# Kernel tuning notes

Hardware: AMD Instinct MI355X
Metric: run time of the kernel (lower is better)

Reference implementation:

```python
import jax, jax.numpy as jnp
import numpy as np

HEADS = 20
HEAD_DIM = 64  # 1280 / 20
IP_SCALE = 1.0


def _split_heads(x, B):
    # [B, S, H*D] -> [B, H, S, D]
    return x.reshape(B, -1, HEADS, HEAD_DIM).transpose(0, 2, 1, 3)


def _merge_heads(x, B):
    # [B, H, S, D] -> [B, S, H*D]
    return x.transpose(0, 2, 1, 3).reshape(B, -1, HEADS * HEAD_DIM)


def _sdpa(q, k, v):
    # q:[B,H,Sq,D] k,v:[B,H,Sk,D]
    scale = 1.0 / jnp.sqrt(jnp.asarray(HEAD_DIM, q.dtype))
    scores = jnp.einsum('bhqd,bhkd->bhqk', q, k) * scale
    probs = jax.nn.softmax(scores, axis=-1)
    return jnp.einsum('bhqk,bhkd->bhqd', probs, v)


def setup_inputs() -> dict:
    key = jax.random.key(0)
    ks = jax.random.split(key, 10)
    B, S, D = 8, 4096, 1280
    Ctx, Cdim = 77, 2048
    Adim = 768
    inp = {
        'hidden_states': jax.random.normal(ks[0], (B, S, D), jnp.float32),
        'encoder_hidden_states': jax.random.normal(ks[1], (B, Ctx, Cdim), jnp.float32),
        'adapter_embeds': jax.random.normal(ks[2], (B, 1, Adim), jnp.float32),
        'Wq': jax.random.normal(ks[3], (D, D), jnp.float32) * 0.02,
        'Wk': jax.random.normal(ks[4], (Cdim, D), jnp.float32) * 0.02,
        'Wv': jax.random.normal(ks[5], (Cdim, D), jnp.float32) * 0.02,
        'Wk_adapter': jax.random.normal(ks[6], (Adim, D), jnp.float32) * 0.02,
        'Wv_adapter': jax.random.normal(ks[7], (Adim, D), jnp.float32) * 0.02,
        'Wo': jax.random.normal(ks[8], (D, D), jnp.float32) * 0.02,
        'bo': jnp.zeros((D,), jnp.float32),
    }
    return inp


def reference(hidden_states, encoder_hidden_states, adapter_embeds,
              Wq, Wk, Wv, Wk_adapter, Wv_adapter, Wo, bo):
    B = hidden_states.shape[0]

    # base cross-attention projections
    q = _split_heads(hidden_states @ Wq, B)                 # [B,H,S,D]
    k = _split_heads(encoder_hidden_states @ Wk, B)         # [B,H,77,D]
    v = _split_heads(encoder_hidden_states @ Wv, B)
    out = _merge_heads(_sdpa(q, k, v), B)                   # [B,S,H*D]

    # IP-adapter branch: single-token K/V, shares the same query
    k_ip = _split_heads(adapter_embeds @ Wk_adapter, B)     # [B,H,1,D]
    v_ip = _split_heads(adapter_embeds @ Wv_adapter, B)
    out_ip = _merge_heads(_sdpa(q, k_ip, v_ip), B)

    merged = out + IP_SCALE * out_ip
    return merged @ Wo + bo
```

## Files before the change

### kernel.cpp

```cpp
#include <hip/hip_runtime.h>
#include <hip/hip_bf16.h>
#include <cstdint>
#include <cstddef>

typedef __hip_bfloat16 bf16_t;
typedef __attribute__((ext_vector_type(8))) __bf16 bf16x8;
typedef __attribute__((ext_vector_type(4))) float f32x4;

__device__ __forceinline__ void gld_lds16(const void* g, void* l) {
    __builtin_amdgcn_global_load_lds(
        (const __attribute__((address_space(1))) void*)(g),
        (__attribute__((address_space(3))) void*)(l), 16, 0, 0);
}

__global__ void k_cast(const float* __restrict__ in, bf16_t* __restrict__ out, long n) {
    long i = ((long)blockIdx.x * blockDim.x + threadIdx.x) * 4;
    if (i >= n) return;
    float4 v = *(const float4*)(in + i);
    out[i + 0] = __float2bfloat16(v.x);
    out[i + 1] = __float2bfloat16(v.y);
    out[i + 2] = __float2bfloat16(v.z);
    out[i + 3] = __float2bfloat16(v.w);
}

__global__ void k_cast_pad(const float* __restrict__ in, bf16_t* __restrict__ out,
                           int rows_in, int rows_out, int cols) {
    long i = ((long)blockIdx.x * blockDim.x + threadIdx.x) * 4;
    long n = (long)rows_out * cols;
    if (i >= n) return;
    int r = (int)(i / cols);
    if (r < rows_in) {
        float4 v = *(const float4*)(in + i);
        out[i + 0] = __float2bfloat16(v.x);
        out[i + 1] = __float2bfloat16(v.y);
        out[i + 2] = __float2bfloat16(v.z);
        out[i + 3] = __float2bfloat16(v.w);
    } else {
        bf16_t z = __float2bfloat16(0.f);
        out[i + 0] = z; out[i + 1] = z; out[i + 2] = z; out[i + 3] = z;
    }
}

__global__ void k_transpose_cast(const float* __restrict__ in, bf16_t* __restrict__ out,
                                 int R, int C) {
    __shared__ float tile[32][33];
    int bx = blockIdx.x * 32;
    int by = blockIdx.y * 32;
    int tx = threadIdx.x & 31, ty = threadIdx.x >> 5;
    #pragma unroll
    for (int j = 0; j < 32; j += 8)
        tile[ty + j][tx] = in[(size_t)(by + ty + j) * C + bx + tx];
    __syncthreads();
    #pragma unroll
    for (int j = 0; j < 32; j += 8)
        out[(size_t)(bx + ty + j) * R + by + tx] = __float2bfloat16(tile[tx][ty + j]);
}

__global__ void k_adapter(const float* __restrict__ ae, const float* __restrict__ Wva,
                          float* __restrict__ vip) {
    int g = blockIdx.x * 256 + threadIdx.x;
    int b = g / 1280, n = g % 1280;
    const float* a = ae + b * 768;
    float acc = 0.f;
    for (int k = 0; k < 768; ++k) acc += a[k] * Wva[(size_t)k * 1280 + n];
    vip[g] = acc;
}

template <bool OUT_BF16, bool ADD_BIAS, bool SWZ>
__global__ __launch_bounds__(256, 2) void k_gemm_bt(
    const bf16_t* __restrict__ A, const bf16_t* __restrict__ Bt,
    void* __restrict__ Cv, const float* __restrict__ bias, int M, int N, int K,
    int snt, int mtx) {
    __shared__ __align__(16) bf16_t As[128 * 32];
    __shared__ __align__(16) bf16_t Bs[128 * 32];
    const int tid = threadIdx.x;
    int m0, n0;
    if constexpr (SWZ) {
        int id = blockIdx.x;
        int xcd = id & 7, j = id >> 3;
        m0 = (xcd * mtx + j / snt) * 128;
        n0 = (j % snt) * 128;
    } else {
        m0 = blockIdx.y * 128;
        n0 = blockIdx.x * 128;
    }
    const int wave = tid >> 6, lane = tid & 63;
    const int wm = (wave >> 1) * 64, wn = (wave & 1) * 64;
    const int quad = lane >> 4, l16 = lane & 15;

    f32x4 acc[4][4] = {};

    const int c0 = tid, c1 = tid + 256;
    const int r0 = c0 >> 2, o0 = (c0 & 3) * 8;
    const int r1 = c1 >> 2, o1 = (c1 & 3) * 8;
    const bf16_t* a0 = A + (size_t)(m0 + r0) * K + o0;
    const bf16_t* a1 = A + (size_t)(m0 + r1) * K + o1;
    const bf16_t* b0 = Bt + (size_t)(n0 + r0) * K + o0;
    const bf16_t* b1 = Bt + (size_t)(n0 + r1) * K + o1;

    for (int k0 = 0; k0 < K; k0 += 32) {
        __syncthreads();
        gld_lds16(a0 + k0, As + c0 * 8);
        gld_lds16(a1 + k0, As + c1 * 8);
        gld_lds16(b0 + k0, Bs + c0 * 8);
        gld_lds16(b1 + k0, Bs + c1 * 8);
        __syncthreads();
        bf16x8 af[4], bfv[4];
        #pragma unroll
        for (int t = 0; t < 4; ++t) {
            af[t]  = *(const bf16x8*)(As + (wm + t * 16 + l16) * 32 + quad * 8);
            bfv[t] = *(const bf16x8*)(Bs + (wn + t * 16 + l16) * 32 + quad * 8);
        }
        #pragma unroll
        for (int mt = 0; mt < 4; ++mt)
            #pragma unroll
            for (int nt = 0; nt < 4; ++nt)
                acc[mt][nt] = __builtin_amdgcn_mfma_f32_16x16x32_bf16(af[mt], bfv[nt], acc[mt][nt], 0, 0, 0);
    }

    if constexpr (OUT_BF16) {
        bf16_t* C = (bf16_t*)Cv;
        #pragma unroll
        for (int mt = 0; mt < 4; ++mt)
            #pragma unroll
            for (int rg = 0; rg < 4; ++rg) {
                int row = m0 + wm + mt * 16 + quad * 4 + rg;
                #pragma unroll
                for (int nt = 0; nt < 4; ++nt) {
                    int col = n0 + wn + nt * 16 + l16;
                    C[(size_t)row * N + col] = __float2bfloat16(acc[mt][nt][rg]);
                }
            }
    } else {
        float* C = (float*)Cv;
        float bv[4];
        #pragma unroll
        for (int nt = 0; nt < 4; ++nt)
            bv[nt] = ADD_BIAS ? bias[n0 + wn + nt * 16 + l16] : 0.f;
        #pragma unroll
        for (int mt = 0; mt < 4; ++mt)
            #pragma unroll
            for (int rg = 0; rg < 4; ++rg) {
                int row = m0 + wm + mt * 16 + quad * 4 + rg;
                #pragma unroll
                for (int nt = 0; nt < 4; ++nt) {
                    int col = n0 + wn + nt * 16 + l16;
                    C[(size_t)row * N + col] = acc[mt][nt][rg] + bv[nt];
                }
            }
    }
}

__global__ __launch_bounds__(256, 2) void k_attn(
    const bf16_t* __restrict__ Q, const bf16_t* __restrict__ Kc,
    const bf16_t* __restrict__ Vc, const float* __restrict__ vip,
    bf16_t* __restrict__ Mrg) {
    __shared__ __align__(16) bf16_t Qs[128 * 64];
    __shared__ __align__(16) bf16_t Ks[96 * 64];
    __shared__ __align__(16) bf16_t Vt[64 * 96];
    __shared__ __align__(16) bf16_t Ps[128 * 96];
    const int tid = threadIdx.x;
    const int qb = blockIdx.x, h = blockIdx.y, b = blockIdx.z;
    const int wave = tid >> 6, lane = tid & 63;
    const int quad = lane >> 4, l16 = lane & 15;

    const bf16_t* Qg = Q + ((size_t)(b * 4096 + qb * 128)) * 1280 + h * 64;
    #pragma unroll
    for (int j = 0; j < 4; ++j) {
        int c = tid + j * 256;
        int r = c >> 3, o = (c & 7) * 8;
        gld_lds16(Qg + (size_t)r * 1280 + o, Qs + c * 8);
    }
    bf16_t z = __float2bfloat16(0.f);
    for (int i = 77 * 64 + tid; i < 96 * 64; i += 256) Ks[i] = z;
    for (int i = tid; i < 64 * 19; i += 256) {
        int d = i / 19, kk = 77 + i % 19;
        Vt[d * 96 + kk] = z;
    }
    for (int c = tid; c < 616; c += 256) {
        int r = c >> 3, o = (c & 7) * 8;
        size_t gi = ((size_t)(b * 77 + r)) * 1280 + h * 64 + o;
        int4 kv = *(const int4*)(Kc + gi);
        *(int4*)(Ks + r * 64 + o) = kv;
        int4 vv = *(const int4*)(Vc + gi);
        const bf16_t* ve = (const bf16_t*)&vv;
        #pragma unroll
        for (int j = 0; j < 8; ++j) Vt[(o + j) * 96 + r] = ve[j];
    }
    __syncthreads();

    f32x4 sacc[2][6] = {};
    #pragma unroll
    for (int ks = 0; ks < 2; ++ks) {
        bf16x8 aq[2], bk[6];
        #pragma unroll
        for (int mt = 0; mt < 2; ++mt)
            aq[mt] = *(const bf16x8*)(Qs + (wave * 32 + mt * 16 + l16) * 64 + ks * 32 + quad * 8);
        #pragma unroll
        for (int nt = 0; nt < 6; ++nt)
            bk[nt] = *(const bf16x8*)(Ks + (nt * 16 + l16) * 64 + ks * 32 + quad * 8);
        #pragma unroll
        for (int mt = 0; mt < 2; ++mt)
            #pragma unroll
            for (int nt = 0; nt < 6; ++nt)
                sacc[mt][nt] = __builtin_amdgcn_mfma_f32_16x16x32_bf16(aq[mt], bk[nt], sacc[mt][nt], 0, 0, 0);
    }
    #pragma unroll
    for (int mt = 0; mt < 2; ++mt)
        #pragma unroll
        for (int nt = 0; nt < 6; ++nt)
            #pragma unroll
            for (int rg = 0; rg < 4; ++rg) {
                int row = wave * 32 + mt * 16 + quad * 4 + rg;
                int col = nt * 16 + l16;
                Ps[row * 96 + col] = __float2bfloat16(sacc[mt][nt][rg] * 0.125f);
            }
    __syncthreads();

    {
        int row = tid >> 1, half = tid & 1;
        int cbeg = half ? 39 : 0, cend = half ? 77 : 39;
        bf16_t* prow = Ps + row * 96;
        float mx = -1e30f;
        for (int c = cbeg; c < cend; ++c) mx = fmaxf(mx, __bfloat162float(prow[c]));
        mx = fmaxf(mx, __shfl_xor(mx, 1));
        float sm = 0.f;
        for (int c = cbeg; c < cend; ++c) sm += __expf(__bfloat162float(prow[c]) - mx);
        sm += __shfl_xor(sm, 1);
        float inv = 1.f / sm;
        for (int c = cbeg; c < cend; ++c)
            prow[c] = __float2bfloat16(__expf(__bfloat162float(prow[c]) - mx) * inv);
    }
    __syncthreads();

    f32x4 oacc[2][4] = {};
    #pragma unroll
    for (int ks = 0; ks < 3; ++ks) {
        bf16x8 ap[2], bv[4];
        #pragma unroll
        for (int mt = 0; mt < 2; ++mt)
            ap[mt] = *(const bf16x8*)(Ps + (wave * 32 + mt * 16 + l16) * 96 + ks * 32 + quad * 8);
        #pragma unroll
        for (int nt = 0; nt < 4; ++nt)
            bv[nt] = *(const bf16x8*)(Vt + (nt * 16 + l16) * 96 + ks * 32 + quad * 8);
        #pragma unroll
        for (int mt = 0; mt < 2; ++mt)
            #pragma unroll
            for (int nt = 0; nt < 4; ++nt)
                oacc[mt][nt] = __builtin_amdgcn_mfma_f32_16x16x32_bf16(ap[mt], bv[nt], oacc[mt][nt], 0, 0, 0);
    }
    #pragma unroll
    for (int nt = 0; nt < 4; ++nt) {
        int col = nt * 16 + l16;
        float add = vip[b * 1280 + h * 64 + col];
        #pragma unroll
        for (int mt = 0; mt < 2; ++mt)
            #pragma unroll
            for (int rg = 0; rg < 4; ++rg) {
                int row = wave * 32 + mt * 16 + quad * 4 + rg;
                Mrg[((size_t)(b * 4096 + qb * 128 + row)) * 1280 + h * 64 + col] =
                    __float2bfloat16(oacc[mt][nt][rg] + add);
            }
    }
}

extern "C" void kernel_launch(void* const* d_in, const int* in_sizes, int n_in,
                              void* d_out, int out_size, void* d_ws, size_t ws_size,
                              hipStream_t stream) {
    (void)in_sizes; (void)n_in; (void)out_size; (void)ws_size;
    const float* hs  = (const float*)d_in[0];
    const float* enc = (const float*)d_in[1];
    const float* ae  = (const float*)d_in[2];
    const float* Wq  = (const float*)d_in[3];
    const float* Wk  = (const float*)d_in[4];
    const float* Wv  = (const float*)d_in[5];
    const float* Wva = (const float*)d_in[7];
    const float* Wo  = (const float*)d_in[8];
    const float* bo  = (const float*)d_in[9];
    float* out = (float*)d_out;

    char* ws = (char*)d_ws;
    size_t off = 0;
    auto alloc = [&](size_t bytes) -> void* {
        void* p = ws + off;
        off += (bytes + 255) & ~(size_t)255;
        return p;
    };
    bf16_t* Xb  = (bf16_t*)alloc((size_t)32768 * 1280 * 2);
    bf16_t* Qb  = (bf16_t*)alloc((size_t)32768 * 1280 * 2);
    bf16_t* Mrg = (bf16_t*)alloc((size_t)32768 * 1280 * 2);
    bf16_t* Eb  = (bf16_t*)alloc((size_t)640 * 2048 * 2);
    bf16_t* WqT = (bf16_t*)alloc((size_t)1280 * 1280 * 2);
    bf16_t* WkT = (bf16_t*)alloc((size_t)1280 * 2048 * 2);
    bf16_t* WvT = (bf16_t*)alloc((size_t)1280 * 2048 * 2);
    bf16_t* WoT = (bf16_t*)alloc((size_t)1280 * 1280 * 2);
    bf16_t* Kc  = (bf16_t*)alloc((size_t)640 * 1280 * 2);
    bf16_t* Vc  = (bf16_t*)alloc((size_t)640 * 1280 * 2);
    float*  vip = (float*)alloc((size_t)8 * 1280 * 4);

    k_cast<<<40960, 256, 0, stream>>>(hs, Xb, (long)32768 * 1280);
    k_cast_pad<<<1280, 256, 0, stream>>>(enc, Eb, 616, 640, 2048);
    k_transpose_cast<<<dim3(40, 40), 256, 0, stream>>>(Wq, WqT, 1280, 1280);
    k_transpose_cast<<<dim3(40, 64), 256, 0, stream>>>(Wk, WkT, 2048, 1280);
    k_transpose_cast<<<dim3(40, 64), 256, 0, stream>>>(Wv, WvT, 2048, 1280);
    k_transpose_cast<<<dim3(40, 40), 256, 0, stream>>>(Wo, WoT, 1280, 1280);
    k_adapter<<<40, 256, 0, stream>>>(ae, Wva, vip);

    k_gemm_bt<true, false, true><<<2560, 256, 0, stream>>>(Xb, WqT, Qb, nullptr, 32768, 1280, 1280, 10, 32);
    k_gemm_bt<true, false, false><<<dim3(10, 5), 256, 0, stream>>>(Eb, WkT, Kc, nullptr, 640, 1280, 2048, 0, 0);
    k_gemm_bt<true, false, false><<<dim3(10, 5), 256, 0, stream>>>(Eb, WvT, Vc, nullptr, 640, 1280, 2048, 0, 0);

    k_attn<<<dim3(32, 20, 8), 256, 0, stream>>>(Qb, Kc, Vc, vip, Mrg);

    k_gemm_bt<false, true, true><<<2560, 256, 0, stream>>>(Mrg, WoT, out, bo, 32768, 1280, 1280, 10, 32);
}
```

Baseline: 864.5 us.

## Add 256x256-tile pipelined GEMM for Q and output projections

Adds a new GEMM kernel with 256x256 tiles and 512 threads, double-buffered LDS staging through global_load_lds, XOR-swizzled shared layout, and interleaved quarter-tile MFMA phases with barriers and raised priority. The large Q projection and output projection now use it instead of the 128-tile kernel, with XCD-aware block mapping. Bigger tiles raise arithmetic intensity and cut global traffic, while the staged schedule tries to overlap loads with MFMA. In exchange it uses much more LDS and registers per block, which lowers occupancy, and the hand-tuned waitcnt scheduling is fragile.

```diff
diff --git a/kernel.cpp b/kernel.cpp
--- a/kernel.cpp
+++ b/kernel.cpp
@@ -145,6 +145,187 @@
                 #pragma unroll
                 for (int nt = 0; nt < 4; ++nt) {
                     int col = n0 + wn + nt * 16 + l16;
+                    C[(size_t)row * N + col] = acc[mt][nt][rg] + bv[nt];
+                }
+            }
+    }
+}
+
+template <bool OUT_BF16, bool ADD_BIAS>
+__global__ __launch_bounds__(512, 2) void k_gemm256(
+    const bf16_t* __restrict__ A, const bf16_t* __restrict__ Bt,
+    void* __restrict__ Cv, const float* __restrict__ bias,
+    int M, int N, int K, int snt, int mtx) {
+    (void)M;
+    __shared__ __align__(16) bf16_t As[2][256 * 64];
+    __shared__ __align__(16) bf16_t Bs[2][256 * 64];
+    const int tid = threadIdx.x;
+    const int id = blockIdx.x;
+    const int xcd = id & 7, jb = id >> 3;
+    const int m0 = (xcd * mtx + jb / snt) * 256;
+    const int n0 = (jb % snt) * 256;
+    const int wave = tid >> 6, lane = tid & 63;
+    const int wm = wave >> 2, wn = wave & 3;
+    const int quad = lane >> 4, l16 = lane & 15;
+
+    const int lr0 = tid >> 3;
+    const int cst = ((tid & 7) * 8) ^ ((lr0 & 7) * 8);
+    const bf16_t* pA0 = A + (size_t)(m0 + lr0) * K + cst;
+    const bf16_t* pA1 = pA0 + (size_t)128 * K;
+    const bf16_t* pB0 = Bt + (size_t)(n0 + ((lr0 >> 5) << 6) + (lr0 & 31)) * K + cst;
+    const bf16_t* pB1 = pB0 + (size_t)128 * K;
+    const int eA0 = tid * 8, eA1 = 4096 + tid * 8;
+
+    const int xorc = (l16 & 7) * 8;
+    const int c0x = (quad * 8) ^ xorc;
+    const int c1x = (32 + quad * 8) ^ xorc;
+    const int arow = (wm * 64 + l16) * 64;
+    const int brow = (wn * 32 + l16) * 64;
+
+    f32x4 acc[8][4] = {};
+    bf16x8 af[4][2], bfr[4][2];
+
+#define STAGE_A_(WB, MH, KT) do { \
+    size_t ko_ = (size_t)(KT) * 64 + (size_t)(MH) * 64 * K; \
+    gld_lds16(pA0 + ko_, &As[WB][(MH) * 8192 + eA0]); \
+    gld_lds16(pA1 + ko_, &As[WB][(MH) * 8192 + eA1]); } while (0)
+#define STAGE_B_(WB, NH, KT) do { \
+    size_t ko_ = (size_t)(KT) * 64 + (size_t)(NH) * 32 * K; \
+    gld_lds16(pB0 + ko_, &Bs[WB][(NH) * 8192 + eA0]); \
+    gld_lds16(pB1 + ko_, &Bs[WB][(NH) * 8192 + eA1]); } while (0)
+#define LOAD_A_(RB, MH) do { _Pragma("unroll") \
+    for (int mt = 0; mt < 4; ++mt) { \
+      const bf16_t* p_ = &As[RB][(MH) * 8192 + arow + mt * 1024]; \
+      af[mt][0] = *(const bf16x8*)(p_ + c0x); \
+      af[mt][1] = *(const bf16x8*)(p_ + c1x); } } while (0)
+#define LOAD_B_(RB, NH) do { _Pragma("unroll") \
+    for (int nt = 0; nt < 2; ++nt) { \
+      const bf16_t* p_ = &Bs[RB][(NH) * 8192 + brow + nt * 1024]; \
+      bfr[(NH) * 2 + nt][0] = *(const bf16x8*)(p_ + c0x); \
+      bfr[(NH) * 2 + nt][1] = *(const bf16x8*)(p_ + c1x); } } while (0)
+#define MMA_(MH, NH) do { _Pragma("unroll") \
+    for (int mt = 0; mt < 4; ++mt) _Pragma("unroll") \
+    for (int nt = 0; nt < 2; ++nt) _Pragma("unroll") \
+    for (int ks = 0; ks < 2; ++ks) \
+      acc[(MH) * 4 + mt][(NH) * 2 + nt] = __builtin_amdgcn_mfma_f32_16x16x32_bf16( \
+          af[mt][ks], bfr[(NH) * 2 + nt][ks], acc[(MH) * 4 + mt][(NH) * 2 + nt], 0, 0, 0); } while (0)
+#define BARRIER_ asm volatile("s_barrier" ::: "memory")
+#define WAITL0_ do { asm volatile("s_waitcnt lgkmcnt(0)" ::: "memory"); \
+    __builtin_amdgcn_sched_barrier(0); } while (0)
+
+#define TILEFULL(T, RB) do { \
+    LOAD_A_(RB, 0); LOAD_B_(RB, 0); \
+    STAGE_A_((RB) ^ 1, 1, (T) + 1); \
+    asm volatile("s_waitcnt lgkmcnt(8)" ::: "memory"); \
+    BARRIER_; WAITL0_; \
+    __builtin_amdgcn_s_setprio(1); MMA_(0, 0); __builtin_amdgcn_s_setprio(0); \
+    BARRIER_; \
+    LOAD_B_(RB, 1); \
+    STAGE_A_(RB, 0, (T) + 2); \
+    BARRIER_; WAITL0_; \
+    __builtin_amdgcn_s_setprio(1); MMA_(0, 1); __builtin_amdgcn_s_setprio(0); \
+    BARRIER_; \
+    LOAD_A_(RB, 1); \
+    STAGE_B_(RB, 0, (T) + 2); \
+    BARRIER_; WAITL0_; \
+    __builtin_amdgcn_s_setprio(1); MMA_(1, 0); __builtin_amdgcn_s_setprio(0); \
+    BARRIER_; \
+    STAGE_B_(RB, 1, (T) + 2); \
+    asm volatile("s_waitcnt vmcnt(6)" ::: "memory"); \
+    BARRIER_; \
+    __builtin_amdgcn_s_setprio(1); MMA_(1, 1); __builtin_amdgcn_s_setprio(0); \
+    BARRIER_; \
+  } while (0)
+
+#define TILEEPI(T, RB) do { \
+    LOAD_A_(RB, 0); LOAD_B_(RB, 0); \
+    STAGE_A_((RB) ^ 1, 1, (T) + 1); \
+    asm volatile("s_waitcnt lgkmcnt(8)" ::: "memory"); \
+    BARRIER_; WAITL0_; \
+    __builtin_amdgcn_s_setprio(1); MMA_(0, 0); __builtin_amdgcn_s_setprio(0); \
+    BARRIER_; \
+    LOAD_B_(RB, 1); \
+    BARRIER_; WAITL0_; \
+    __builtin_amdgcn_s_setprio(1); MMA_(0, 1); __builtin_amdgcn_s_setprio(0); \
+    BARRIER_; \
+    LOAD_A_(RB, 1); \
+    BARRIER_; WAITL0_; \
+    __builtin_amdgcn_s_setprio(1); MMA_(1, 0); __builtin_amdgcn_s_setprio(0); \
+    BARRIER_; \
+    asm volatile("s_waitcnt vmcnt(0)" ::: "memory"); \
+    BARRIER_; \
+    __builtin_amdgcn_s_setprio(1); MMA_(1, 1); __builtin_amdgcn_s_setprio(0); \
+    BARRIER_; \
+  } while (0)
+
+#define TILELAST(RB) do { \
+    LOAD_A_(RB, 0); LOAD_B_(RB, 0); \
+    MMA_(0, 0); \
+    LOAD_B_(RB, 1); \
+    MMA_(0, 1); \
+    LOAD_A_(RB, 1); \
+    MMA_(1, 0); \
+    MMA_(1, 1); \
+  } while (0)
+
+    const int NT = K >> 6;
+
+    STAGE_A_(0, 0, 0);
+    STAGE_B_(0, 0, 0);
+    STAGE_B_(0, 1, 0);
+    STAGE_A_(0, 1, 0);
+    STAGE_A_(1, 0, 1);
+    STAGE_B_(1, 0, 1);
+    STAGE_B_(1, 1, 1);
+    asm volatile("s_waitcnt vmcnt(6)" ::: "memory");
+    BARRIER_;
+
+    #pragma unroll 1
+    for (int t = 0; t < NT - 2; t += 2) {
+        TILEFULL(t, 0);
+        TILEFULL(t + 1, 1);
+    }
+    TILEEPI(NT - 2, 0);
+    TILELAST(1);
+
+#undef STAGE_A_
+#undef STAGE_B_
+#undef LOAD_A_
+#undef LOAD_B_
+#undef MMA_
+#undef BARRIER_
+#undef WAITL0_
+#undef TILEFULL
+#undef TILEEPI
+#undef TILELAST
+
+    if constexpr (OUT_BF16) {
+        bf16_t* C = (bf16_t*)Cv;
+        #pragma unroll
+        for (int mt = 0; mt < 8; ++mt)
+            #pragma unroll
+            for (int rg = 0; rg < 4; ++rg) {
+                int row = m0 + wm * 128 + (mt >> 2) * 64 + (mt & 3) * 16 + quad * 4 + rg;
+                #pragma unroll
+                for (int nt = 0; nt < 4; ++nt) {
+                    int col = n0 + wn * 64 + nt * 16 + l16;
+                    C[(size_t)row * N + col] = __float2bfloat16(acc[mt][nt][rg]);
+                }
+            }
+    } else {
+        float* C = (float*)Cv;
+        float bv[4];
+        #pragma unroll
+        for (int nt = 0; nt < 4; ++nt)
+            bv[nt] = ADD_BIAS ? bias[n0 + wn * 64 + nt * 16 + l16] : 0.f;
+        #pragma unroll
+        for (int mt = 0; mt < 8; ++mt)
+            #pragma unroll
+            for (int rg = 0; rg < 4; ++rg) {
+                int row = m0 + wm * 128 + (mt >> 2) * 64 + (mt & 3) * 16 + quad * 4 + rg;
+                #pragma unroll
+                for (int nt = 0; nt < 4; ++nt) {
+                    int col = n0 + wn * 64 + nt * 16 + l16;
                     C[(size_t)row * N + col] = acc[mt][nt][rg] + bv[nt];
                 }
             }
@@ -306,11 +487,11 @@
     k_transpose_cast<<<dim3(40, 40), 256, 0, stream>>>(Wo, WoT, 1280, 1280);
     k_adapter<<<40, 256, 0, stream>>>(ae, Wva, vip);
 
-    k_gemm_bt<true, false, true><<<2560, 256, 0, stream>>>(Xb, WqT, Qb, nullptr, 32768, 1280, 1280, 10, 32);
+    k_gemm256<true, false><<<640, 512, 0, stream>>>(Xb, WqT, Qb, nullptr, 32768, 1280, 1280, 5, 16);
     k_gemm_bt<true, false, false><<<dim3(10, 5), 256, 0, stream>>>(Eb, WkT, Kc, nullptr, 640, 1280, 2048, 0, 0);
     k_gemm_bt<true, false, false><<<dim3(10, 5), 256, 0, stream>>>(Eb, WvT, Vc, nullptr, 640, 1280, 2048, 0, 0);
 
     k_attn<<<dim3(32, 20, 8), 256, 0, stream>>>(Qb, Kc, Vc, vip, Mrg);
 
-    k_gemm_bt<false, true, true><<<2560, 256, 0, stream>>>(Mrg, WoT, out, bo, 32768, 1280, 1280, 10, 32);
-}
+    k_gemm256<false, true><<<640, 512, 0, stream>>>(Mrg, WoT, out, bo, 32768, 1280, 1280, 5, 16);
+}
```

Result: faster. 843.6 us (-2.4%).
